# Kernel optimization log

Measured on AMD Instinct MI355X. Metric: run time of the kernel, lower is better.

The kernel has to match this reference:

```python
import jax, jax.numpy as jnp
import numpy as np

H, DD, NCLS, NELEM, NPROP = 256, 32, 8, 11, 14
B, N = 4, 4096
ENC = NELEM + NPROP  # 25

_DIMS = [("dc1", ENC, H), ("dc21", H, DD), ("dc22", H, DD),
         ("in1", ENC, H), ("in2", H, H), ("in3", H, H),
         ("conv", H, H),
         ("id1", H, H), ("id2", H, H), ("id3", H, H),
         ("oid", H, NCLS), ("och", H, 2),
         ("m1", H + NCLS, H + NCLS), ("m2", H + NCLS, H), ("m3", H, H), ("om", H, 3)]


def setup_inputs() -> dict:
    key = jax.random.key(0)
    ks = jax.random.split(key, 2 + len(_DIMS))
    X = jax.random.normal(ks[0], (B, N, 15), jnp.float32)
    ids = jax.random.randint(ks[1], (B, N), 0, NELEM).astype(jnp.float32)
    X = X.at[:, :, 0].set(ids)
    d = {"X": X}
    for i, (name, di, do) in enumerate(_DIMS):
        W = jax.random.normal(ks[2 + i], (di, do), jnp.float32) / np.sqrt(di)
        d["W_" + name] = W
        d["b_" + name] = jnp.zeros((do,), jnp.float32)
    return d


def reference(X, W_dc1, b_dc1, W_dc21, b_dc21, W_dc22, b_dc22,
              W_in1, b_in1, W_in2, b_in2, W_in3, b_in3,
              W_conv, b_conv,
              W_id1, b_id1, W_id2, b_id2, W_id3, b_id3,
              W_oid, b_oid, W_och, b_och,
              W_m1, b_m1, W_m2, b_m2, W_m3, b_m3, W_om, b_om):
    act = jax.nn.selu
    # input encoding: one-hot element id (stop-grad via int cast) + properties, then selu
    onehot = jax.nn.one_hot(X[:, :, 0].astype(jnp.int32), NELEM, dtype=X.dtype)
    enc = act(jnp.concatenate([onehot, X[:, :, 1:]], axis=-1))  # [B,N,25]
    # distance coordinates
    h = act(enc @ W_dc1 + b_dc1)
    c1 = h @ W_dc21 + b_dc21  # [B,N,DD]
    c2 = h @ W_dc22 + b_dc22
    # pairwise distance -> exp adjacency
    na = jnp.sum(c1 * c1, -1)[:, :, None]
    nb = jnp.sum(c2 * c2, -1)[:, None, :]
    Dsq = jnp.clip(na - 2.0 * jnp.einsum('bnd,bmd->bnm', c1, c2) + nb, 1e-12, 1e12)
    adj = jnp.exp(-jnp.sqrt(Dsq))  # [B,N,N]
    # node MLP
    x = act(enc @ W_in1 + b_in1)
    x = act(x @ W_in2 + b_in2)
    x = act(x @ W_in3 + b_in3)
    # GraphConv: adj^k @ (x W) + b, k=4 (in-degree norm computed but unused upstream)
    x = act(jnp.einsum('bnm,bmh->bnh', adj ** 4, x @ W_conv) + b_conv)
    # id head
    a = act(x @ W_id1 + b_id1)
    a = act(a @ W_id2 + b_id2)
    a = act(a @ W_id3 + b_id3)
    out_id_logits = a @ W_oid + b_oid  # [B,N,8]
    out_charge = a @ W_och + b_och     # [B,N,2]
    # momentum head
    xb = jnp.concatenate([x, act(out_id_logits)], axis=-1)
    bb = act(xb @ W_m1 + b_m1)
    bb = act(bb @ W_m2 + b_m2)
    bb = act(bb @ W_m3 + b_m3)
    corr = bb @ W_om + b_om  # [B,N,3]
    mom = jnp.stack([X[:, :, 2] + corr[:, :, 0],
                     X[:, :, 3] + corr[:, :, 1],
                     X[:, :, 4] + corr[:, :, 2]], axis=-1)
    return jnp.concatenate([out_id_logits, mom, out_charge], axis=-1)  # [B,N,13]
```

## Files before the change

kernel.cpp:

```cpp
#include <hip/hip_runtime.h>
#include <cstddef>
#include <cstdint>

#define MROWS 16384
#define NSEQ  4096
#define ASTR  296
#define SELU_SCALE  1.0507009873554805f
#define SELU_ASCALE 1.7580993408473766f

typedef short bf16x8 __attribute__((ext_vector_type(8)));
typedef float f32x4  __attribute__((ext_vector_type(4)));

__device__ __forceinline__ float selu_f(float x) {
    return x > 0.f ? SELU_SCALE * x : SELU_ASCALE * (__expf(x) - 1.f);
}
__device__ __forceinline__ unsigned short f2bf(float x) {
    union { float f; unsigned int u; } v; v.f = x;
    unsigned int r = v.u + 0x7fffu + ((v.u >> 16) & 1u);
    return (unsigned short)(r >> 16);
}
__device__ __forceinline__ unsigned short t2bf(float x) {
    union { float f; unsigned int u; } v; v.f = x;
    return (unsigned short)(v.u >> 16);
}

struct PrepEnt { const float* W; unsigned short* WTf; int N, K, ntiles, KS, tileOff, tilesN; };
struct PrepArgs {
    PrepEnt e[16];
    const float *b21, *b22, *boid, *boch, *bdc1, *bin1;
    float *bc12, *boo, *bcat;
};
__global__ __launch_bounds__(256) void prep_kernel(PrepArgs pa) {
    if (blockIdx.y == 1) {
        if (blockIdx.x == 0) {
            int t = threadIdx.x;
            if (t < 32) pa.bc12[t] = pa.b21[t];
            else if (t < 64) pa.bc12[t] = pa.b22[t - 32];
            else if (t < 96) {
                int j = t - 64;
                pa.boo[j] = j < 8 ? pa.boid[j] : ((j >= 16 && j < 18) ? pa.boch[j - 16] : 0.f);
            }
        } else if (blockIdx.x == 1) {
            pa.bcat[threadIdx.x] = pa.bdc1[threadIdx.x];
        } else if (blockIdx.x == 2) {
            pa.bcat[256 + threadIdx.x] = pa.bin1[threadIdx.x];
        }
        return;
    }
    int bx = blockIdx.x;
    int ei = 0;
#pragma unroll
    for (int e = 1; e < 16; ++e)
        if (bx >= pa.e[e].tileOff) ei = e;
    PrepEnt E = pa.e[ei];
    int local = bx - E.tileOff;
    int tn = local / E.KS, tk = local - tn * E.KS;
    int k0 = tk * 32, n0 = tn * 32;

    __shared__ float ts[32][33];
    int t = threadIdx.x;
    {
        int kl = t >> 3, nl4 = (t & 7) * 4;
        int gk = k0 + kl;
#pragma unroll
        for (int j = 0; j < 4; ++j) {
            int gn = n0 + nl4 + j;
            float v = (gk < E.K && gn < E.N) ? E.W[(size_t)gk * E.N + gn] : 0.f;
            ts[nl4 + j][kl] = v;
        }
    }
    __syncthreads();
    int nl = t >> 3, kl4 = (t & 7) * 4;
    int n = n0 + nl;
    if (n < E.ntiles * 16) {
        ushort4 o;
        o.x = f2bf(ts[nl][kl4 + 0]);
        o.y = f2bf(ts[nl][kl4 + 1]);
        o.z = f2bf(ts[nl][kl4 + 2]);
        o.w = f2bf(ts[nl][kl4 + 3]);
        size_t dst = ((size_t)(n >> 4) * E.KS + tk) * 512 +
                     (size_t)((kl4 >> 3) * 16 + (n & 15)) * 8 + (kl4 & 7);
        *(ushort4*)(E.WTf + dst) = o;
    }
}

template <int MT, int NT>
__device__ __forceinline__ void zero_acc(f32x4 (&acc)[MT][NT]) {
#pragma unroll
    for (int i = 0; i < MT; ++i)
#pragma unroll
        for (int nt = 0; nt < NT; ++nt) acc[i][nt] = (f32x4){0.f, 0.f, 0.f, 0.f};
}

template <int MT, int NT, int K>
__device__ __forceinline__ void compute_tiles(
    f32x4 (&acc)[MT][NT],
    const unsigned short* __restrict__ src, int sstr,
    const unsigned short* __restrict__ WTf,
    int col0, int ln)
{
    constexpr int KS = (K + 31) / 32;
    int quad = ln >> 4, l15 = ln & 15;
    const unsigned short* wp = WTf + (size_t)(col0 >> 4) * (KS * 512) + ln * 8;
    bf16x8 w[KS][NT];
#pragma unroll
    for (int ks = 0; ks < KS; ++ks)
#pragma unroll
        for (int nt = 0; nt < NT; ++nt)
            w[ks][nt] = *(const bf16x8*)(wp + nt * (KS * 512) + ks * 512);
#pragma unroll
    for (int ks = 0; ks < KS; ++ks) {
#pragma unroll
        for (int i = 0; i < MT; ++i) {
            bf16x8 af = *(const bf16x8*)(src + (i * 16 + l15) * sstr + ks * 32 + quad * 8);
#pragma unroll
            for (int nt = 0; nt < NT; ++nt)
                acc[i][nt] = __builtin_amdgcn_mfma_f32_16x16x32_bf16(af, w[ks][nt], acc[i][nt], 0, 0, 0);
        }
    }
}

template <int MT, int NT>
__device__ __forceinline__ void store_tiles(
    f32x4 (&acc)[MT][NT], unsigned short* __restrict__ dst,
    int col0, const float* __restrict__ bias, int Nreal, int act, int ln)
{
    int quad = ln >> 4, l15 = ln & 15;
#pragma unroll
    for (int nt = 0; nt < NT; ++nt) {
        int col = col0 + nt * 16 + l15;
        float bv = (bias && col < Nreal) ? bias[col] : 0.f;
#pragma unroll
        for (int i = 0; i < MT; ++i) {
#pragma unroll
            for (int r = 0; r < 4; ++r) {
                int row = i * 16 + quad * 4 + r;
                float v = acc[i][nt][r] + bv;
                if (act) v = selu_f(v);
                if (col >= Nreal) v = 0.f;
                dst[row * ASTR + col] = f2bf(v);
            }
        }
    }
}

__global__ __launch_bounds__(256, 2) void pre_mega(
    const float* __restrict__ X,
    const unsigned short* __restrict__ WTdF, const float* __restrict__ bcat,
    const unsigned short* __restrict__ WTc12F, const float* __restrict__ bc12,
    const unsigned short* __restrict__ WTin2F, const float* __restrict__ b_in2,
    const unsigned short* __restrict__ WTin3F, const float* __restrict__ b_in3,
    const unsigned short* __restrict__ WTconvF,
    unsigned short* __restrict__ c1b, unsigned short* __restrict__ c2b,
    float* __restrict__ n1, float* __restrict__ n2,
    unsigned short* __restrict__ xwTb)
{
    __shared__ unsigned short encs[32 * 32];
    __shared__ unsigned short bufA[32 * ASTR];
    __shared__ unsigned short bufB[32 * ASTR];
    __shared__ float c12s[32 * 68];

    int tid = threadIdx.x, wv = tid >> 6, ln = tid & 63;
    int quad = ln >> 4, l15 = ln & 15;
    int row0 = blockIdx.x * 32;

#pragma unroll
    for (int p = 0; p < 4; ++p) {
        int idx = p * 256 + tid;
        int row = idx >> 5, col = idx & 31;
        float v = 0.f;
        if (col < 11) {
            int id = (int)X[(size_t)(row0 + row) * 15];
            v = (id == col) ? SELU_SCALE : 0.f;
        } else if (col < 25) {
            v = selu_f(X[(size_t)(row0 + row) * 15 + 1 + (col - 11)]);
        }
        encs[row * 32 + col] = f2bf(v);
    }
    __syncthreads();

#pragma unroll
    for (int ph = 0; ph < 2; ++ph) {
        f32x4 acc[2][4]; zero_acc<2, 4>(acc);
        compute_tiles<2, 4, 32>(acc, encs, 32, WTdF + (size_t)ph * 16 * 512, wv * 64, ln);
        store_tiles<2, 4>(acc, ph ? bufB : bufA, wv * 64, bcat + ph * 256, 256, 1, ln);
    }
    __syncthreads();

    f32x4 ax2[2][4]; zero_acc<2, 4>(ax2);
    compute_tiles<2, 4, 256>(ax2, bufB, ASTR, WTin2F, wv * 64, ln);
    f32x4 ac12[2][1]; zero_acc<2, 1>(ac12);
    compute_tiles<2, 1, 256>(ac12, bufA, ASTR, WTc12F, wv * 16, ln);
    __syncthreads();
    store_tiles<2, 4>(ax2, bufA, wv * 64, b_in2, 256, 1, ln);
    {
        int col = wv * 16 + l15;
        float bv = bc12[col];
#pragma unroll
        for (int i = 0; i < 2; ++i)
#pragma unroll
            for (int r = 0; r < 4; ++r)
                c12s[(i * 16 + quad * 4 + r) * 68 + col] = ac12[i][0][r] + bv;
    }
    __syncthreads();

    if (tid < 32) {
        int grow = row0 + tid;
        const float* p = &c12s[tid * 68];
        float s1 = 0.f, s2 = 0.f;
        unsigned int o1[16], o2[16];
#pragma unroll
        for (int k = 0; k < 32; k += 2) {
            float a0 = p[k], a1 = p[k + 1];
            s1 += a0 * a0 + a1 * a1;
            o1[k >> 1] = (unsigned)f2bf(a0) | ((unsigned)f2bf(a1) << 16);
            float b0 = p[32 + k], b1 = p[33 + k];
            s2 += b0 * b0 + b1 * b1;
            o2[k >> 1] = (unsigned)f2bf(b0) | ((unsigned)f2bf(b1) << 16);
        }
        uint4* d1 = (uint4*)(c1b + (size_t)grow * 32);
        uint4* d2 = (uint4*)(c2b + (size_t)grow * 32);
#pragma unroll
        for (int j = 0; j < 4; ++j) {
            d1[j] = make_uint4(o1[4 * j], o1[4 * j + 1], o1[4 * j + 2], o1[4 * j + 3]);
            d2[j] = make_uint4(o2[4 * j], o2[4 * j + 1], o2[4 * j + 2], o2[4 * j + 3]);
        }
        n1[grow] = s1;
        n2[grow] = s2;
    }

    {
        f32x4 acc[2][4]; zero_acc<2, 4>(acc);
        compute_tiles<2, 4, 256>(acc, bufA, ASTR, WTin3F, wv * 64, ln);
        store_tiles<2, 4>(acc, bufB, wv * 64, b_in3, 256, 1, ln);
    }
    __syncthreads();
    {
        f32x4 acc[2][4]; zero_acc<2, 4>(acc);
        compute_tiles<2, 4, 256>(acc, bufB, ASTR, WTconvF, wv * 64, ln);
        store_tiles<2, 4>(acc, bufA, wv * 64, nullptr, 256, 0, ln);
    }
    __syncthreads();

    int b = row0 >> 12;
    int c0 = (row0 & 4095) >> 5;
    unsigned short* dst = xwTb + (size_t)(b * 128 + c0) * (256 * 32);
#pragma unroll
    for (int p = 0; p < 4; ++p) {
        int idx = p * 256 + tid;
        int h = idx >> 2, g = idx & 3;
        unsigned int w[4];
#pragma unroll
        for (int j = 0; j < 4; ++j) {
            unsigned int lo = bufA[(g * 8 + 2 * j) * ASTR + h];
            unsigned int hi = bufA[(g * 8 + 2 * j + 1) * ASTR + h];
            w[j] = lo | (hi << 16);
        }
        *(uint4*)(dst + (size_t)h * 32 + g * 8) = make_uint4(w[0], w[1], w[2], w[3]);
    }
}

__global__ __launch_bounds__(512, 4) void adj_conv_mfma(
    const unsigned short* __restrict__ c1b, const unsigned short* __restrict__ c2b,
    const float* __restrict__ n1, const float* __restrict__ n2,
    const unsigned short* __restrict__ xwTb, const float* __restrict__ bconv,
    unsigned short* __restrict__ xc)
{
    __shared__ unsigned short wls[2][32][136];

    int tid = threadIdx.x, wv = tid >> 6, ln = tid & 63, quad = ln >> 4, l15 = ln & 15;
    int blk = blockIdx.x;
    int b = (blk >> 1) & 3;
    int iidx = ((blk >> 3) << 1) | (blk & 1);
    int i0 = iidx * 32;
    size_t base = (size_t)b * NSEQ;

    bf16x8 c1f0 = *(const bf16x8*)(c1b + (base + i0 + l15) * 32 + quad * 8);
    bf16x8 c1f1 = *(const bf16x8*)(c1b + (base + i0 + 16 + l15) * 32 + quad * 8);
    float4 n1v0 = *(const float4*)(n1 + base + i0 + quad * 4);
    float4 n1v1 = *(const float4*)(n1 + base + i0 + 16 + quad * 4);

    const unsigned short* xwp0 = xwTb + (size_t)b * (128 * 256 * 32)
                               + ((size_t)(wv * 32 + l15) * 32 + quad * 8);
    const unsigned short* xwp1 = xwp0 + 8192;
    const unsigned short* xwp2 = xwp0 + 16384;
    const unsigned short* xwp3 = xwp0 + 24576;
    const unsigned short* c2p  = c2b + (base + wv * 16 + l15) * 32 + quad * 8;
    const float* n2p = n2 + base + wv * 16 + l15;

    f32x4 acc[2][2];
#pragma unroll
    for (int i = 0; i < 2; ++i)
#pragma unroll
        for (int j = 0; j < 2; ++j) acc[i][j] = (f32x4){0.f, 0.f, 0.f, 0.f};

    bf16x8 c2f = *(const bf16x8*)c2p;
    float nn2 = *n2p;
    c2p += 4096; n2p += 128;
    {
        f32x4 d0 = (f32x4){0.f, 0.f, 0.f, 0.f};
        f32x4 d1 = (f32x4){0.f, 0.f, 0.f, 0.f};
        d0 = __builtin_amdgcn_mfma_f32_16x16x32_bf16(c1f0, c2f, d0, 0, 0, 0);
        d1 = __builtin_amdgcn_mfma_f32_16x16x32_bf16(c1f1, c2f, d1, 0, 0, 0);
#pragma unroll
        for (int r = 0; r < 4; ++r) {
            float D0 = fmaf(-2.f, d0[r], n1v0[r] + nn2);
            float D1 = fmaf(-2.f, d1[r], n1v1[r] + nn2);
            float t0 = __builtin_amdgcn_sqrtf(fmaxf(D0, 1e-12f));
            float t1 = __builtin_amdgcn_sqrtf(fmaxf(D1, 1e-12f));
            wls[0][quad * 4 + r][wv * 16 + l15]      = t2bf(__expf(t0 * -4.f));
            wls[0][16 + quad * 4 + r][wv * 16 + l15] = t2bf(__expf(t1 * -4.f));
        }
    }
    c2f = *(const bf16x8*)c2p;
    nn2 = *n2p;
    c2p += 4096; n2p += 128;
    __syncthreads();

    for (int itr = 0; itr < 32; ++itr) {
        int p = itr & 1;
        bf16x8 bfc[4][2];
#pragma unroll
        for (int ht = 0; ht < 2; ++ht) {
            bfc[0][ht] = *(const bf16x8*)(xwp0 + ht * 512);
            bfc[1][ht] = *(const bf16x8*)(xwp1 + ht * 512);
            bfc[2][ht] = *(const bf16x8*)(xwp2 + ht * 512);
            bfc[3][ht] = *(const bf16x8*)(xwp3 + ht * 512);
        }
        xwp0 += 32768; xwp1 += 32768; xwp2 += 32768; xwp3 += 32768;

        if (itr < 31) {
            f32x4 d0 = (f32x4){0.f, 0.f, 0.f, 0.f};
            f32x4 d1 = (f32x4){0.f, 0.f, 0.f, 0.f};
            d0 = __builtin_amdgcn_mfma_f32_16x16x32_bf16(c1f0, c2f, d0, 0, 0, 0);
            d1 = __builtin_amdgcn_mfma_f32_16x16x32_bf16(c1f1, c2f, d1, 0, 0, 0);
            bf16x8 c2n; float nnn;
            if (itr < 30) {
                c2n = *(const bf16x8*)c2p;
                nnn = *n2p;
                c2p += 4096; n2p += 128;
            }
#pragma unroll
            for (int r = 0; r < 4; ++r) {
                float D0 = fmaf(-2.f, d0[r], n1v0[r] + nn2);
                float D1 = fmaf(-2.f, d1[r], n1v1[r] + nn2);
                float t0 = __builtin_amdgcn_sqrtf(fmaxf(D0, 1e-12f));
                float t1 = __builtin_amdgcn_sqrtf(fmaxf(D1, 1e-12f));
                wls[p ^ 1][quad * 4 + r][wv * 16 + l15]      = t2bf(__expf(t0 * -4.f));
                wls[p ^ 1][16 + quad * 4 + r][wv * 16 + l15] = t2bf(__expf(t1 * -4.f));
            }
            if (itr < 30) { c2f = c2n; nn2 = nnn; }
        }

#pragma unroll
        for (int ks = 0; ks < 4; ++ks) {
            bf16x8 af0 = *(const bf16x8*)&wls[p][l15][ks * 32 + quad * 8];
            bf16x8 af1 = *(const bf16x8*)&wls[p][16 + l15][ks * 32 + quad * 8];
            acc[0][0] = __builtin_amdgcn_mfma_f32_16x16x32_bf16(af0, bfc[ks][0], acc[0][0], 0, 0, 0);
            acc[0][1] = __builtin_amdgcn_mfma_f32_16x16x32_bf16(af0, bfc[ks][1], acc[0][1], 0, 0, 0);
            acc[1][0] = __builtin_amdgcn_mfma_f32_16x16x32_bf16(af1, bfc[ks][0], acc[1][0], 0, 0, 0);
            acc[1][1] = __builtin_amdgcn_mfma_f32_16x16x32_bf16(af1, bfc[ks][1], acc[1][1], 0, 0, 0);
        }
        __syncthreads();
    }

#pragma unroll
    for (int mi = 0; mi < 2; ++mi) {
#pragma unroll
        for (int ht = 0; ht < 2; ++ht) {
            int h = wv * 32 + ht * 16 + l15;
            float bv = bconv[h];
#pragma unroll
            for (int r = 0; r < 4; ++r) {
                int irow = i0 + mi * 16 + quad * 4 + r;
                xc[(base + irow) * 256 + h] = f2bf(selu_f(acc[mi][ht][r] + bv));
            }
        }
    }
}

__global__ __launch_bounds__(256, 2) void post_mega(
    const float* __restrict__ X, const unsigned short* __restrict__ xc,
    const unsigned short* __restrict__ WTid1F, const float* __restrict__ b_id1,
    const unsigned short* __restrict__ WTid2F, const float* __restrict__ b_id2,
    const unsigned short* __restrict__ WTid3F, const float* __restrict__ b_id3,
    const unsigned short* __restrict__ WTooF, const float* __restrict__ boo,
    const unsigned short* __restrict__ WTm1F, const float* __restrict__ b_m1,
    const unsigned short* __restrict__ WTm2F, const float* __restrict__ b_m2,
    const unsigned short* __restrict__ WTm3F, const float* __restrict__ b_m3,
    const unsigned short* __restrict__ WTomF, const float* __restrict__ b_om,
    float* __restrict__ out)
{
    __shared__ unsigned short xcs[32 * ASTR];
    __shared__ unsigned short bufA[32 * ASTR];
    __shared__ unsigned short bufB[32 * ASTR];
    __shared__ float lgs[32 * 32];

    int tid = threadIdx.x, wv = tid >> 6, ln = tid & 63;
    int quad = ln >> 4, l15 = ln & 15;
    int row0 = blockIdx.x * 32;

#pragma unroll
    for (int p = 0; p < 4; ++p) {
        int idx = p * 256 + tid;
        int row = idx >> 5, c8 = (idx & 31) * 8;
        *(uint4*)&xcs[row * ASTR + c8] = *(const uint4*)(xc + (size_t)(row0 + row) * 256 + c8);
    }
#pragma unroll
    for (int p = 0; p < 5; ++p) {
        int idx = p * 256 + tid;
        int row = idx / 40, c = 256 + idx - row * 40;
        xcs[row * ASTR + c] = 0;
        bufB[row * ASTR + c] = 0;
    }
    __syncthreads();

    {
        f32x4 acc[2][4]; zero_acc<2, 4>(acc);
        compute_tiles<2, 4, 256>(acc, xcs, ASTR, WTid1F, wv * 64, ln);
        store_tiles<2, 4>(acc, bufA, wv * 64, b_id1, 256, 1, ln);
    }
    __syncthreads();
    {
        f32x4 acc[2][4]; zero_acc<2, 4>(acc);
        compute_tiles<2, 4, 256>(acc, bufA, ASTR, WTid2F, wv * 64, ln);
        store_tiles<2, 4>(acc, bufB, wv * 64, b_id2, 256, 1, ln);
    }
    __syncthreads();
    {
        f32x4 acc[2][4]; zero_acc<2, 4>(acc);
        compute_tiles<2, 4, 256>(acc, bufB, ASTR, WTid3F, wv * 64, ln);
        store_tiles<2, 4>(acc, bufA, wv * 64, b_id3, 256, 1, ln);
    }
    __syncthreads();
    if (wv == 0) {
        f32x4 acc[2][2]; zero_acc<2, 2>(acc);
        compute_tiles<2, 2, 256>(acc, bufA, ASTR, WTooF, 0, ln);
#pragma unroll
        for (int nt = 0; nt < 2; ++nt) {
            int col = nt * 16 + l15;
            float bv = boo[col];
#pragma unroll
            for (int i = 0; i < 2; ++i)
#pragma unroll
                for (int r = 0; r < 4; ++r)
                    lgs[(i * 16 + quad * 4 + r) * 32 + col] = acc[i][nt][r] + bv;
        }
    }
    __syncthreads();
    if (tid < 32) {
        float* op = out + (size_t)(row0 + tid) * 13;
#pragma unroll
        for (int c = 0; c < 8; ++c) {
            float lg = lgs[tid * 32 + c];
            op[c] = lg;
            xcs[tid * ASTR + 256 + c] = f2bf(selu_f(lg));
        }
        op[11] = lgs[tid * 32 + 16];
        op[12] = lgs[tid * 32 + 17];
    }
    __syncthreads();
    {
        f32x4 acc[2][4]; zero_acc<2, 4>(acc);
        compute_tiles<2, 4, 288>(acc, xcs, ASTR, WTm1F, wv * 64, ln);
        store_tiles<2, 4>(acc, bufB, wv * 64, b_m1, 264, 1, ln);
        if (wv == 1) {
            f32x4 acx[2][1]; zero_acc<2, 1>(acx);
            compute_tiles<2, 1, 288>(acx, xcs, ASTR, WTm1F, 256, ln);
            store_tiles<2, 1>(acx, bufB, 256, b_m1, 264, 1, ln);
        }
    }
    __syncthreads();
    {
        f32x4 acc[2][4]; zero_acc<2, 4>(acc);
        compute_tiles<2, 4, 288>(acc, bufB, ASTR, WTm2F, wv * 64, ln);
        store_tiles<2, 4>(acc, bufA, wv * 64, b_m2, 256, 1, ln);
    }
    __syncthreads();
    {
        f32x4 acc[2][4]; zero_acc<2, 4>(acc);
        compute_tiles<2, 4, 256>(acc, bufA, ASTR, WTm3F, wv * 64, ln);
        store_tiles<2, 4>(acc, bufB, wv * 64, b_m3, 256, 1, ln);
    }
    __syncthreads();
    if (wv == 0) {
        f32x4 acc[2][1]; zero_acc<2, 1>(acc);
        compute_tiles<2, 1, 256>(acc, bufB, ASTR, WTomF, 0, ln);
        if (l15 < 3) {
            float bv = b_om[l15];
#pragma unroll
            for (int i = 0; i < 2; ++i)
#pragma unroll
                for (int r = 0; r < 4; ++r) {
                    int grow = row0 + i * 16 + quad * 4 + r;
                    out[(size_t)grow * 13 + 8 + l15] =
                        X[(size_t)grow * 15 + 2 + l15] + acc[i][0][r] + bv;
                }
        }
    }
}

extern "C" void kernel_launch(void* const* d_in, const int* in_sizes, int n_in,
                              void* d_out, int out_size, void* d_ws, size_t ws_size,
                              hipStream_t stream) {
    (void)in_sizes; (void)n_in; (void)out_size; (void)ws_size;

    const float* X = (const float*)d_in[0];
    const float* W_dc1 = (const float*)d_in[1];  const float* b_dc1 = (const float*)d_in[2];
    const float* W_dc21 = (const float*)d_in[3]; const float* b_dc21 = (const float*)d_in[4];
    const float* W_dc22 = (const float*)d_in[5]; const float* b_dc22 = (const float*)d_in[6];
    const float* W_in1 = (const float*)d_in[7];  const float* b_in1 = (const float*)d_in[8];
    const float* W_in2 = (const float*)d_in[9];  const float* b_in2 = (const float*)d_in[10];
    const float* W_in3 = (const float*)d_in[11]; const float* b_in3 = (const float*)d_in[12];
    const float* W_conv = (const float*)d_in[13]; const float* b_conv = (const float*)d_in[14];
    const float* W_id1 = (const float*)d_in[15]; const float* b_id1 = (const float*)d_in[16];
    const float* W_id2 = (const float*)d_in[17]; const float* b_id2 = (const float*)d_in[18];
    const float* W_id3 = (const float*)d_in[19]; const float* b_id3 = (const float*)d_in[20];
    const float* W_oid = (const float*)d_in[21]; const float* b_oid = (const float*)d_in[22];
    const float* W_och = (const float*)d_in[23]; const float* b_och = (const float*)d_in[24];
    const float* W_m1 = (const float*)d_in[25];  const float* b_m1 = (const float*)d_in[26];
    const float* W_m2 = (const float*)d_in[27];  const float* b_m2 = (const float*)d_in[28];
    const float* W_m3 = (const float*)d_in[29];  const float* b_m3 = (const float*)d_in[30];
    const float* W_om = (const float*)d_in[31];  const float* b_om = (const float*)d_in[32];

    const size_t M = MROWS;
    char* pw = (char*)d_ws;
    auto alloc = [&](size_t bytes) -> void* {
        void* r = (void*)pw;
        pw += (bytes + 255) & ~(size_t)255;
        return r;
    };
    unsigned short* c1b = (unsigned short*)alloc(M * 32 * 2);
    unsigned short* c2b = (unsigned short*)alloc(M * 32 * 2);
    float* n1 = (float*)alloc(M * 4);
    float* n2 = (float*)alloc(M * 4);
    unsigned short* xwTb = (unsigned short*)alloc((size_t)4 * 128 * 256 * 32 * 2);
    unsigned short* xcb = (unsigned short*)alloc(M * 256 * 2);
    unsigned short* WTdF   = (unsigned short*)alloc((size_t)2 * 16 * 1 * 512 * 2);
    unsigned short* WTc12F = (unsigned short*)alloc((size_t)4 * 8 * 512 * 2);
    unsigned short* WTin2F = (unsigned short*)alloc((size_t)16 * 8 * 512 * 2);
    unsigned short* WTin3F = (unsigned short*)alloc((size_t)16 * 8 * 512 * 2);
    unsigned short* WTconvF = (unsigned short*)alloc((size_t)16 * 8 * 512 * 2);
    unsigned short* WTid1F = (unsigned short*)alloc((size_t)16 * 8 * 512 * 2);
    unsigned short* WTid2F = (unsigned short*)alloc((size_t)16 * 8 * 512 * 2);
    unsigned short* WTid3F = (unsigned short*)alloc((size_t)16 * 8 * 512 * 2);
    unsigned short* WTm3F  = (unsigned short*)alloc((size_t)16 * 8 * 512 * 2);
    unsigned short* WTooF  = (unsigned short*)alloc((size_t)2 * 8 * 512 * 2);
    unsigned short* WTm1F  = (unsigned short*)alloc((size_t)17 * 9 * 512 * 2);
    unsigned short* WTm2F  = (unsigned short*)alloc((size_t)16 * 9 * 512 * 2);
    unsigned short* WTomF  = (unsigned short*)alloc((size_t)1 * 8 * 512 * 2);
    float* bc12 = (float*)alloc(64 * 4);
    float* boo = (float*)alloc(32 * 4);
    float* bcat = (float*)alloc(512 * 4);

    PrepArgs pa;
    int off = 0;
    auto ent = [&](const float* W, unsigned short* WTf, int N, int K, int ntiles) {
        PrepEnt e; e.W = W; e.WTf = WTf; e.N = N; e.K = K; e.ntiles = ntiles;
        e.KS = (K + 31) / 32;
        e.tilesN = (ntiles * 16 + 31) / 32;
        e.tileOff = off;
        off += e.tilesN * e.KS;
        return e;
    };
    pa.e[0]  = ent(W_dc1,  WTdF,                256, 25,  16);
    pa.e[1]  = ent(W_in1,  WTdF + 16 * 512,     256, 25,  16);
    pa.e[2]  = ent(W_dc21, WTc12F,              32,  256, 2);
    pa.e[3]  = ent(W_dc22, WTc12F + 2 * 8 * 512, 32, 256, 2);
    pa.e[4]  = ent(W_in2,  WTin2F,              256, 256, 16);
    pa.e[5]  = ent(W_in3,  WTin3F,              256, 256, 16);
    pa.e[6]  = ent(W_conv, WTconvF,             256, 256, 16);
    pa.e[7]  = ent(W_id1,  WTid1F,              256, 256, 16);
    pa.e[8]  = ent(W_id2,  WTid2F,              256, 256, 16);
    pa.e[9]  = ent(W_id3,  WTid3F,              256, 256, 16);
    pa.e[10] = ent(W_m3,   WTm3F,               256, 256, 16);
    pa.e[11] = ent(W_oid,  WTooF,               8,   256, 1);
    pa.e[12] = ent(W_och,  WTooF + 8 * 512,     2,   256, 1);
    pa.e[13] = ent(W_m1,   WTm1F,               264, 264, 17);
    pa.e[14] = ent(W_m2,   WTm2F,               256, 264, 16);
    pa.e[15] = ent(W_om,   WTomF,               3,   256, 1);
    pa.b21 = b_dc21; pa.b22 = b_dc22; pa.boid = b_oid; pa.boch = b_och;
    pa.bdc1 = b_dc1; pa.bin1 = b_in1;
    pa.bc12 = bc12; pa.boo = boo; pa.bcat = bcat;
    prep_kernel<<<dim3(off, 2), 256, 0, stream>>>(pa);

    pre_mega<<<dim3(512), 256, 0, stream>>>(X, WTdF, bcat, WTc12F, bc12,
                                            WTin2F, b_in2, WTin3F, b_in3, WTconvF,
                                            c1b, c2b, n1, n2, xwTb);

    adj_conv_mfma<<<dim3(512), 512, 0, stream>>>(c1b, c2b, n1, n2, xwTb, b_conv, xcb);

    post_mega<<<dim3(512), 256, 0, stream>>>(X, xcb,
                                             WTid1F, b_id1, WTid2F, b_id2, WTid3F, b_id3,
                                             WTooF, boo, WTm1F, b_m1, WTm2F, b_m2,
                                             WTm3F, b_m3, WTomF, b_om, (float*)d_out);
}
```

Measured before the change: 252.6 us.

## Make pre/post MLP kernels wave-independent over 16-row tiles without block barriers

Each wave in the pre and post MLP kernels now owns a private 16-row slice with its own LDS ping-pong buffers. It computes every output column for that slice, so all __syncthreads calls between layers go away. Weights are streamed per 16-column tile with a three-deep register rotation, and each block now covers 64 rows, which halves the grid to 256 blocks with launch bounds of 1 block per CU. The aim is to cut barrier stalls and per-block overhead. The cost is that every wave reads the full weight matrix (four times more weight traffic per block), fewer blocks are in flight, and a larger LDS footprint may limit occupancy.

```diff
diff --git a/kernel.cpp b/kernel.cpp
--- a/kernel.cpp
+++ b/kernel.cpp
@@ -84,67 +84,96 @@
     }
 }
 
-template <int MT, int NT>
-__device__ __forceinline__ void zero_acc(f32x4 (&acc)[MT][NT]) {
-#pragma unroll
-    for (int i = 0; i < MT; ++i)
-#pragma unroll
-        for (int nt = 0; nt < NT; ++nt) acc[i][nt] = (f32x4){0.f, 0.f, 0.f, 0.f};
-}
-
-template <int MT, int NT, int K>
-__device__ __forceinline__ void compute_tiles(
-    f32x4 (&acc)[MT][NT],
-    const unsigned short* __restrict__ src, int sstr,
-    const unsigned short* __restrict__ WTf,
-    int col0, int ln)
-{
-    constexpr int KS = (K + 31) / 32;
-    int quad = ln >> 4, l15 = ln & 15;
-    const unsigned short* wp = WTf + (size_t)(col0 >> 4) * (KS * 512) + ln * 8;
-    bf16x8 w[KS][NT];
-#pragma unroll
-    for (int ks = 0; ks < KS; ++ks)
-#pragma unroll
-        for (int nt = 0; nt < NT; ++nt)
-            w[ks][nt] = *(const bf16x8*)(wp + nt * (KS * 512) + ks * 512);
-#pragma unroll
-    for (int ks = 0; ks < KS; ++ks) {
-#pragma unroll
-        for (int i = 0; i < MT; ++i) {
-            bf16x8 af = *(const bf16x8*)(src + (i * 16 + l15) * sstr + ks * 32 + quad * 8);
-#pragma unroll
-            for (int nt = 0; nt < NT; ++nt)
-                acc[i][nt] = __builtin_amdgcn_mfma_f32_16x16x32_bf16(af, w[ks][nt], acc[i][nt], 0, 0, 0);
-        }
-    }
-}
-
-template <int MT, int NT>
-__device__ __forceinline__ void store_tiles(
-    f32x4 (&acc)[MT][NT], unsigned short* __restrict__ dst,
-    int col0, const float* __restrict__ bias, int Nreal, int act, int ln)
+template <int KS, int NTT>
+__device__ __forceinline__ void wave_layer(
+    const unsigned short* sbuf, unsigned short* dbuf,
+    const unsigned short* WTf, const float* bias, int Nreal, int act, int ln)
 {
     int quad = ln >> 4, l15 = ln & 15;
-#pragma unroll
-    for (int nt = 0; nt < NT; ++nt) {
-        int col = col0 + nt * 16 + l15;
+    bf16x8 af[KS];
+#pragma unroll
+    for (int ks = 0; ks < KS; ++ks)
+        af[ks] = *(const bf16x8*)(sbuf + l15 * ASTR + ks * 32 + quad * 8);
+    const unsigned short* wp = WTf + ln * 8;
+    f32x4 acc[NTT];
+#pragma unroll
+    for (int nt = 0; nt < NTT; ++nt) acc[nt] = (f32x4){0.f, 0.f, 0.f, 0.f};
+
+    bf16x8 w[3][KS];
+#pragma unroll
+    for (int s = 0; s < 3; ++s) {
+        if (s < NTT) {
+#pragma unroll
+            for (int ks = 0; ks < KS; ++ks)
+                w[s][ks] = *(const bf16x8*)(wp + (size_t)s * (KS * 512) + ks * 512);
+        }
+    }
+#pragma unroll
+    for (int nt = 0; nt < NTT; ++nt) {
+        bf16x8 wn[KS];
+        if (nt + 3 < NTT) {
+#pragma unroll
+            for (int ks = 0; ks < KS; ++ks)
+                wn[ks] = *(const bf16x8*)(wp + (size_t)(nt + 3) * (KS * 512) + ks * 512);
+        }
+#pragma unroll
+        for (int ks = 0; ks < KS; ++ks)
+            acc[nt] = __builtin_amdgcn_mfma_f32_16x16x32_bf16(af[ks], w[nt % 3][ks], acc[nt], 0, 0, 0);
+        if (nt + 3 < NTT) {
+#pragma unroll
+            for (int ks = 0; ks < KS; ++ks) w[nt % 3][ks] = wn[ks];
+        }
+    }
+#pragma unroll
+    for (int nt = 0; nt < NTT; ++nt) {
+        int col = nt * 16 + l15;
         float bv = (bias && col < Nreal) ? bias[col] : 0.f;
 #pragma unroll
-        for (int i = 0; i < MT; ++i) {
-#pragma unroll
-            for (int r = 0; r < 4; ++r) {
-                int row = i * 16 + quad * 4 + r;
-                float v = acc[i][nt][r] + bv;
-                if (act) v = selu_f(v);
-                if (col >= Nreal) v = 0.f;
-                dst[row * ASTR + col] = f2bf(v);
-            }
-        }
-    }
-}
-
-__global__ __launch_bounds__(256, 2) void pre_mega(
+        for (int r = 0; r < 4; ++r) {
+            int row = quad * 4 + r;
+            float v = acc[nt][r] + bv;
+            if (act) v = selu_f(v);
+            if (col >= Nreal) v = 0.f;
+            dbuf[row * ASTR + col] = f2bf(v);
+        }
+    }
+}
+
+template <int KS, int NTT>
+__device__ __forceinline__ void wave_layer_f32(
+    const unsigned short* sbuf, float* fdst, int fstride,
+    const unsigned short* WTf, const float* bias, int ln)
+{
+    int quad = ln >> 4, l15 = ln & 15;
+    bf16x8 af[KS];
+#pragma unroll
+    for (int ks = 0; ks < KS; ++ks)
+        af[ks] = *(const bf16x8*)(sbuf + l15 * ASTR + ks * 32 + quad * 8);
+    const unsigned short* wp = WTf + ln * 8;
+    f32x4 acc[NTT];
+#pragma unroll
+    for (int nt = 0; nt < NTT; ++nt) acc[nt] = (f32x4){0.f, 0.f, 0.f, 0.f};
+#pragma unroll
+    for (int nt = 0; nt < NTT; ++nt) {
+        bf16x8 w[KS];
+#pragma unroll
+        for (int ks = 0; ks < KS; ++ks)
+            w[ks] = *(const bf16x8*)(wp + (size_t)nt * (KS * 512) + ks * 512);
+#pragma unroll
+        for (int ks = 0; ks < KS; ++ks)
+            acc[nt] = __builtin_amdgcn_mfma_f32_16x16x32_bf16(af[ks], w[ks], acc[nt], 0, 0, 0);
+    }
+#pragma unroll
+    for (int nt = 0; nt < NTT; ++nt) {
+        int col = nt * 16 + l15;
+        float bv = bias ? bias[col] : 0.f;
+#pragma unroll
+        for (int r = 0; r < 4; ++r)
+            fdst[(quad * 4 + r) * fstride + col] = acc[nt][r] + bv;
+    }
+}
+
+__global__ __launch_bounds__(256, 1) void pre_mega(
     const float* __restrict__ X,
     const unsigned short* __restrict__ WTdF, const float* __restrict__ bcat,
     const unsigned short* __restrict__ WTc12F, const float* __restrict__ bc12,
@@ -155,58 +184,36 @@
     float* __restrict__ n1, float* __restrict__ n2,
     unsigned short* __restrict__ xwTb)
 {
-    __shared__ unsigned short encs[32 * 32];
-    __shared__ unsigned short bufA[32 * ASTR];
-    __shared__ unsigned short bufB[32 * ASTR];
-    __shared__ float c12s[32 * 68];
+    __shared__ unsigned short bufs[4][2][16 * ASTR];
+    __shared__ float c12s[4][16 * 68];
 
     int tid = threadIdx.x, wv = tid >> 6, ln = tid & 63;
-    int quad = ln >> 4, l15 = ln & 15;
-    int row0 = blockIdx.x * 32;
-
-#pragma unroll
-    for (int p = 0; p < 4; ++p) {
-        int idx = p * 256 + tid;
-        int row = idx >> 5, col = idx & 31;
-        float v = 0.f;
-        if (col < 11) {
-            int id = (int)X[(size_t)(row0 + row) * 15];
-            v = (id == col) ? SELU_SCALE : 0.f;
-        } else if (col < 25) {
-            v = selu_f(X[(size_t)(row0 + row) * 15 + 1 + (col - 11)]);
-        }
-        encs[row * 32 + col] = f2bf(v);
-    }
-    __syncthreads();
-
-#pragma unroll
-    for (int ph = 0; ph < 2; ++ph) {
-        f32x4 acc[2][4]; zero_acc<2, 4>(acc);
-        compute_tiles<2, 4, 32>(acc, encs, 32, WTdF + (size_t)ph * 16 * 512, wv * 64, ln);
-        store_tiles<2, 4>(acc, ph ? bufB : bufA, wv * 64, bcat + ph * 256, 256, 1, ln);
-    }
-    __syncthreads();
-
-    f32x4 ax2[2][4]; zero_acc<2, 4>(ax2);
-    compute_tiles<2, 4, 256>(ax2, bufB, ASTR, WTin2F, wv * 64, ln);
-    f32x4 ac12[2][1]; zero_acc<2, 1>(ac12);
-    compute_tiles<2, 1, 256>(ac12, bufA, ASTR, WTc12F, wv * 16, ln);
-    __syncthreads();
-    store_tiles<2, 4>(ax2, bufA, wv * 64, b_in2, 256, 1, ln);
+    int rowbase = blockIdx.x * 64 + wv * 16;
+    unsigned short* A = &bufs[wv][0][0];
+    unsigned short* B = &bufs[wv][1][0];
+    float* c12w = &c12s[wv][0];
+
     {
-        int col = wv * 16 + l15;
-        float bv = bc12[col];
-#pragma unroll
-        for (int i = 0; i < 2; ++i)
-#pragma unroll
-            for (int r = 0; r < 4; ++r)
-                c12s[(i * 16 + quad * 4 + r) * 68 + col] = ac12[i][0][r] + bv;
-    }
-    __syncthreads();
-
-    if (tid < 32) {
-        int grow = row0 + tid;
-        const float* p = &c12s[tid * 68];
+        int row = ln >> 2, c0 = (ln & 3) * 8;
+        const float* xp = X + (size_t)(rowbase + row) * 15;
+        int id = (int)xp[0];
+#pragma unroll
+        for (int j = 0; j < 8; ++j) {
+            int col = c0 + j;
+            float v = 0.f;
+            if (col < 11) v = (id == col) ? SELU_SCALE : 0.f;
+            else if (col < 25) v = selu_f(xp[1 + (col - 11)]);
+            A[row * ASTR + col] = f2bf(v);
+        }
+    }
+
+    wave_layer<1, 16>(A, B, WTdF, bcat, 256, 1, ln);
+    wave_layer<1, 16>(A, A, WTdF + (size_t)16 * 512, bcat + 256, 256, 1, ln);
+    wave_layer_f32<8, 4>(B, c12w, 68, WTc12F, bc12, ln);
+
+    if (ln < 16) {
+        int grow = rowbase + ln;
+        const float* p = &c12w[ln * 68];
         float s1 = 0.f, s2 = 0.f;
         unsigned int o1[16], o2[16];
 #pragma unroll
@@ -229,34 +236,28 @@
         n2[grow] = s2;
     }
 
+    wave_layer<8, 16>(A, B, WTin2F, b_in2, 256, 1, ln);
+    wave_layer<8, 16>(B, A, WTin3F, b_in3, 256, 1, ln);
+    wave_layer<8, 16>(A, B, WTconvF, nullptr, 256, 0, ln);
+
     {
-        f32x4 acc[2][4]; zero_acc<2, 4>(acc);
-        compute_tiles<2, 4, 256>(acc, bufA, ASTR, WTin3F, wv * 64, ln);
-        store_tiles<2, 4>(acc, bufB, wv * 64, b_in3, 256, 1, ln);
-    }
-    __syncthreads();
-    {
-        f32x4 acc[2][4]; zero_acc<2, 4>(acc);
-        compute_tiles<2, 4, 256>(acc, bufB, ASTR, WTconvF, wv * 64, ln);
-        store_tiles<2, 4>(acc, bufA, wv * 64, nullptr, 256, 0, ln);
-    }
-    __syncthreads();
-
-    int b = row0 >> 12;
-    int c0 = (row0 & 4095) >> 5;
-    unsigned short* dst = xwTb + (size_t)(b * 128 + c0) * (256 * 32);
-#pragma unroll
-    for (int p = 0; p < 4; ++p) {
-        int idx = p * 256 + tid;
-        int h = idx >> 2, g = idx & 3;
-        unsigned int w[4];
-#pragma unroll
-        for (int j = 0; j < 4; ++j) {
-            unsigned int lo = bufA[(g * 8 + 2 * j) * ASTR + h];
-            unsigned int hi = bufA[(g * 8 + 2 * j + 1) * ASTR + h];
-            w[j] = lo | (hi << 16);
-        }
-        *(uint4*)(dst + (size_t)h * 32 + g * 8) = make_uint4(w[0], w[1], w[2], w[3]);
+        int b = rowbase >> 12;
+        int chunk = (rowbase & 4095) >> 5;
+        int moff = rowbase & 31;
+        unsigned short* dst = xwTb + (size_t)(b * 128 + chunk) * (256 * 32) + moff;
+#pragma unroll
+        for (int p = 0; p < 8; ++p) {
+            int idx = p * 64 + ln;
+            int h = idx >> 1, g = idx & 1;
+            unsigned int w[4];
+#pragma unroll
+            for (int j = 0; j < 4; ++j) {
+                unsigned int lo = B[(g * 8 + 2 * j) * ASTR + h];
+                unsigned int hi = B[(g * 8 + 2 * j + 1) * ASTR + h];
+                w[j] = lo | (hi << 16);
+            }
+            *(uint4*)(dst + (size_t)h * 32 + g * 8) = make_uint4(w[0], w[1], w[2], w[3]);
+        }
     }
 }
 
@@ -379,7 +380,7 @@
     }
 }
 
-__global__ __launch_bounds__(256, 2) void post_mega(
+__global__ __launch_bounds__(256, 1) void post_mega(
     const float* __restrict__ X, const unsigned short* __restrict__ xc,
     const unsigned short* __restrict__ WTid1F, const float* __restrict__ b_id1,
     const unsigned short* __restrict__ WTid2F, const float* __restrict__ b_id2,
@@ -391,111 +392,72 @@
     const unsigned short* __restrict__ WTomF, const float* __restrict__ b_om,
     float* __restrict__ out)
 {
-    __shared__ unsigned short xcs[32 * ASTR];
-    __shared__ unsigned short bufA[32 * ASTR];
-    __shared__ unsigned short bufB[32 * ASTR];
-    __shared__ float lgs[32 * 32];
+    __shared__ unsigned short bufs[4][2][16 * ASTR];
+    __shared__ float lgs[4][16 * 32];
 
     int tid = threadIdx.x, wv = tid >> 6, ln = tid & 63;
     int quad = ln >> 4, l15 = ln & 15;
-    int row0 = blockIdx.x * 32;
-
-#pragma unroll
-    for (int p = 0; p < 4; ++p) {
-        int idx = p * 256 + tid;
-        int row = idx >> 5, c8 = (idx & 31) * 8;
-        *(uint4*)&xcs[row * ASTR + c8] = *(const uint4*)(xc + (size_t)(row0 + row) * 256 + c8);
-    }
-#pragma unroll
-    for (int p = 0; p < 5; ++p) {
-        int idx = p * 256 + tid;
+    int rowbase = blockIdx.x * 64 + wv * 16;
+    unsigned short* A = &bufs[wv][0][0];
+    unsigned short* B = &bufs[wv][1][0];
+    float* lgw = &lgs[wv][0];
+
+#pragma unroll
+    for (int p = 0; p < 8; ++p) {
+        int idx = p * 64 + ln;
+        int row = idx >> 5, g = idx & 31;
+        *(uint4*)&A[row * ASTR + g * 8] =
+            *(const uint4*)(xc + (size_t)(rowbase + row) * 256 + g * 8);
+    }
+#pragma unroll
+    for (int p = 0; p < 10; ++p) {
+        int idx = p * 64 + ln;
         int row = idx / 40, c = 256 + idx - row * 40;
-        xcs[row * ASTR + c] = 0;
-        bufB[row * ASTR + c] = 0;
-    }
-    __syncthreads();
+        A[row * ASTR + c] = 0;
+        B[row * ASTR + c] = 0;
+    }
+
+    wave_layer<8, 16>(A, B, WTid1F, b_id1, 256, 1, ln);
+    wave_layer<8, 16>(B, B, WTid2F, b_id2, 256, 1, ln);
+    wave_layer<8, 16>(B, B, WTid3F, b_id3, 256, 1, ln);
+    wave_layer_f32<8, 2>(B, lgw, 32, WTooF, boo, ln);
+
+    if (ln < 16) {
+        float* op = out + (size_t)(rowbase + ln) * 13;
+#pragma unroll
+        for (int c = 0; c < 8; ++c) {
+            float lg = lgw[ln * 32 + c];
+            op[c] = lg;
+            A[ln * ASTR + 256 + c] = f2bf(selu_f(lg));
+        }
+        op[11] = lgw[ln * 32 + 16];
+        op[12] = lgw[ln * 32 + 17];
+    }
+
+    wave_layer<9, 17>(A, B, WTm1F, b_m1, 264, 1, ln);
+    wave_layer<9, 16>(B, B, WTm2F, b_m2, 256, 1, ln);
+    wave_layer<8, 16>(B, B, WTm3F, b_m3, 256, 1, ln);
 
     {
-        f32x4 acc[2][4]; zero_acc<2, 4>(acc);
-        compute_tiles<2, 4, 256>(acc, xcs, ASTR, WTid1F, wv * 64, ln);
-        store_tiles<2, 4>(acc, bufA, wv * 64, b_id1, 256, 1, ln);
-    }
-    __syncthreads();
-    {
-        f32x4 acc[2][4]; zero_acc<2, 4>(acc);
-        compute_tiles<2, 4, 256>(acc, bufA, ASTR, WTid2F, wv * 64, ln);
-        store_tiles<2, 4>(acc, bufB, wv * 64, b_id2, 256, 1, ln);
-    }
-    __syncthreads();
-    {
-        f32x4 acc[2][4]; zero_acc<2, 4>(acc);
-        compute_tiles<2, 4, 256>(acc, bufB, ASTR, WTid3F, wv * 64, ln);
-        store_tiles<2, 4>(acc, bufA, wv * 64, b_id3, 256, 1, ln);
-    }
-    __syncthreads();
-    if (wv == 0) {
-        f32x4 acc[2][2]; zero_acc<2, 2>(acc);
-        compute_tiles<2, 2, 256>(acc, bufA, ASTR, WTooF, 0, ln);
-#pragma unroll
-        for (int nt = 0; nt < 2; ++nt) {
-            int col = nt * 16 + l15;
-            float bv = boo[col];
-#pragma unroll
-            for (int i = 0; i < 2; ++i)
-#pragma unroll
-                for (int r = 0; r < 4; ++r)
-                    lgs[(i * 16 + quad * 4 + r) * 32 + col] = acc[i][nt][r] + bv;
-        }
-    }
-    __syncthreads();
-    if (tid < 32) {
-        float* op = out + (size_t)(row0 + tid) * 13;
-#pragma unroll
-        for (int c = 0; c < 8; ++c) {
-            float lg = lgs[tid * 32 + c];
-            op[c] = lg;
-            xcs[tid * ASTR + 256 + c] = f2bf(selu_f(lg));
-        }
-        op[11] = lgs[tid * 32 + 16];
-        op[12] = lgs[tid * 32 + 17];
-    }
-    __syncthreads();
-    {
-        f32x4 acc[2][4]; zero_acc<2, 4>(acc);
-        compute_tiles<2, 4, 288>(acc, xcs, ASTR, WTm1F, wv * 64, ln);
-        store_tiles<2, 4>(acc, bufB, wv * 64, b_m1, 264, 1, ln);
-        if (wv == 1) {
-            f32x4 acx[2][1]; zero_acc<2, 1>(acx);
-            compute_tiles<2, 1, 288>(acx, xcs, ASTR, WTm1F, 256, ln);
-            store_tiles<2, 1>(acx, bufB, 256, b_m1, 264, 1, ln);
-        }
-    }
-    __syncthreads();
-    {
-        f32x4 acc[2][4]; zero_acc<2, 4>(acc);
-        compute_tiles<2, 4, 288>(acc, bufB, ASTR, WTm2F, wv * 64, ln);
-        store_tiles<2, 4>(acc, bufA, wv * 64, b_m2, 256, 1, ln);
-    }
-    __syncthreads();
-    {
-        f32x4 acc[2][4]; zero_acc<2, 4>(acc);
-        compute_tiles<2, 4, 256>(acc, bufA, ASTR, WTm3F, wv * 64, ln);
-        store_tiles<2, 4>(acc, bufB, wv * 64, b_m3, 256, 1, ln);
-    }
-    __syncthreads();
-    if (wv == 0) {
-        f32x4 acc[2][1]; zero_acc<2, 1>(acc);
-        compute_tiles<2, 1, 256>(acc, bufB, ASTR, WTomF, 0, ln);
+        bf16x8 af[8];
+#pragma unroll
+        for (int ks = 0; ks < 8; ++ks)
+            af[ks] = *(const bf16x8*)(B + l15 * ASTR + ks * 32 + quad * 8);
+        const unsigned short* wp = WTomF + ln * 8;
+        f32x4 acc = (f32x4){0.f, 0.f, 0.f, 0.f};
+#pragma unroll
+        for (int ks = 0; ks < 8; ++ks) {
+            bf16x8 w = *(const bf16x8*)(wp + ks * 512);
+            acc = __builtin_amdgcn_mfma_f32_16x16x32_bf16(af[ks], w, acc, 0, 0, 0);
+        }
         if (l15 < 3) {
             float bv = b_om[l15];
 #pragma unroll
-            for (int i = 0; i < 2; ++i)
-#pragma unroll
-                for (int r = 0; r < 4; ++r) {
-                    int grow = row0 + i * 16 + quad * 4 + r;
-                    out[(size_t)grow * 13 + 8 + l15] =
-                        X[(size_t)grow * 15 + 2 + l15] + acc[i][0][r] + bv;
-                }
+            for (int r = 0; r < 4; ++r) {
+                int grow = rowbase + quad * 4 + r;
+                out[(size_t)grow * 13 + 8 + l15] =
+                    X[(size_t)grow * 15 + 2 + l15] + acc[r] + bv;
+            }
         }
     }
 }
@@ -584,13 +546,13 @@
     pa.bc12 = bc12; pa.boo = boo; pa.bcat = bcat;
     prep_kernel<<<dim3(off, 2), 256, 0, stream>>>(pa);
 
-    pre_mega<<<dim3(512), 256, 0, stream>>>(X, WTdF, bcat, WTc12F, bc12,
+    pre_mega<<<dim3(256), 256, 0, stream>>>(X, WTdF, bcat, WTc12F, bc12,
                                             WTin2F, b_in2, WTin3F, b_in3, WTconvF,
                                             c1b, c2b, n1, n2, xwTb);
 
     adj_conv_mfma<<<dim3(512), 512, 0, stream>>>(c1b, c2b, n1, n2, xwTb, b_conv, xcb);
 
-    post_mega<<<dim3(512), 256, 0, stream>>>(X, xcb,
+    post_mega<<<dim3(256), 256, 0, stream>>>(X, xcb,
                                              WTid1F, b_id1, WTid2F, b_id2, WTid3F, b_id3,
                                              WTooF, boo, WTm1F, b_m1, WTm2F, b_m2,
                                              WTm3F, b_m3, WTomF, b_om, (float*)d_out);
```

Measured after the change: 374.9 us. +48.4%, slower.
